# Kernel optimization log

Hardware: AMD Instinct MI355X
Metric: run time of the kernel (lower is better)

Reference implementation:

```python
import jax, jax.numpy as jnp
import numpy as np

HIDDEN = 64
N_NODES = 100000
N_EDGES = 1250000
EDGE_FEAT = 13


def setup_inputs() -> dict:
    key = jax.random.key(0)
    ks = jax.random.split(key, 16)
    d = HIDDEN
    inp = {
        'x': jax.random.normal(ks[0], (N_NODES, d), dtype=jnp.float32),
        'edge_index': jax.random.randint(ks[1], (2, N_EDGES), 0, N_NODES, dtype=jnp.int64),
        'edge_attr': jax.random.uniform(ks[2], (N_EDGES, EDGE_FEAT), dtype=jnp.float32),
        # learned params
        'aaaaa': jax.random.normal(ks[3], (EDGE_FEAT, 1), dtype=jnp.float32) * 0.5,
        'W1': jax.random.normal(ks[4], (d, d), dtype=jnp.float32) / np.sqrt(d),
        'b1': jnp.zeros((d,), dtype=jnp.float32),
        'W2': jax.random.normal(ks[5], (d, d), dtype=jnp.float32) / np.sqrt(d),
        'b2': jnp.zeros((d,), dtype=jnp.float32),
        'W3': jax.random.normal(ks[6], (d, d), dtype=jnp.float32) / np.sqrt(d),
        'b3': jnp.zeros((d,), dtype=jnp.float32),
        'wg1': jax.random.normal(ks[7], (d, 1), dtype=jnp.float32) / np.sqrt(d),
        'bg1': jnp.zeros((1,), dtype=jnp.float32),
        'wg2': jax.random.normal(ks[8], (d, 1), dtype=jnp.float32) / np.sqrt(d),
        'bg2': jnp.zeros((1,), dtype=jnp.float32),
        'wg3': jax.random.normal(ks[9], (d, 1), dtype=jnp.float32) / np.sqrt(d),
        'bg3': jnp.zeros((1,), dtype=jnp.float32),
    }
    return inp


def _gcn_norm(edge_index, edge_weight, num_nodes):
    # PyG gcn_norm: add self-loops (weight 1), symmetric deg^{-1/2} normalization
    loop = jnp.arange(num_nodes, dtype=edge_index.dtype)
    rows = jnp.concatenate([edge_index[0], loop])
    cols = jnp.concatenate([edge_index[1], loop])
    w = jnp.concatenate([edge_weight, jnp.ones((num_nodes,), edge_weight.dtype)])
    deg = jax.ops.segment_sum(w, cols, num_segments=num_nodes)
    dinv = jnp.where(deg > 0, jax.lax.rsqrt(jnp.where(deg > 0, deg, 1.0)), 0.0)
    norm = dinv[rows] * w * dinv[cols]
    return rows, cols, norm


def _gcn_layer(x, W, b, rows, cols, norm, num_nodes):
    h = x @ W  # transform first (out_dim == in_dim)
    msg = norm[:, None] * h[rows]          # gather + scale  [E+N, d]
    out = jnp.zeros_like(h).at[cols].add(msg)  # scatter-add aggregation
    return out + b


def _att_pool(x, wg, bg):
    # GlobalAttention with single graph (batch all zeros):
    # gate = sigmoid(Linear(x)); softmax over nodes; weighted sum
    gate = jax.nn.sigmoid(x @ wg + bg)      # [N, 1]
    a = jax.nn.softmax(gate, axis=0)        # softmax over node dim
    return jnp.sum(a * x, axis=0, keepdims=True)  # [1, d]


def reference(x, edge_index, edge_attr, aaaaa, W1, b1, W2, b2, W3, b3,
              wg1, bg1, wg2, bg2, wg3, bg3):
    num_nodes = x.shape[0]
    edge_weight = (edge_attr @ jax.nn.softmax(aaaaa, axis=0)).reshape(-1)  # [E]
    rows, cols, norm = _gcn_norm(edge_index, edge_weight, num_nodes)

    x1 = jax.nn.relu(_gcn_layer(x, W1, b1, rows, cols, norm, num_nodes))
    r1 = _att_pool(x1, wg1, bg1)
    x2 = jax.nn.relu(_gcn_layer(x1, W2, b2, rows, cols, norm, num_nodes))
    r2 = _att_pool(x2, wg2, bg2)
    x3 = jax.nn.relu(_gcn_layer(x2, W3, b3, rows, cols, norm, num_nodes))
    r3 = _att_pool(x3, wg3, bg3)
    return jnp.concatenate([r1, r2, r3], axis=1)  # [1, 3*hidden]
```

## Files before the change

### kernel.cpp

```cpp
#include <hip/hip_runtime.h>
#include <hip/hip_bf16.h>
#include <math.h>

#define HIDDEN    64
#define N_NODES   100000
#define N_EDGES   1250000
#define EDGE_FEAT 13

#define GATHER_BLOCKS 2048
#define GEMM_NB   ((N_NODES + 255) / 256)

#define NBKT    391
#define BCAP    4096
#define A_EPB   2048
#define NBLKA   ((N_EDGES + A_EPB - 1) / A_EPB)

typedef unsigned short bf16_t;
typedef unsigned char  u8;
typedef unsigned short u16;
typedef unsigned int   u32;
typedef unsigned long long u64;
typedef float f32x2 __attribute__((ext_vector_type(2)));

#if defined(__has_builtin)
# if __has_builtin(__builtin_amdgcn_cvt_f32_fp8)
#  define USE_HW_FP8 1
# endif
# if __has_builtin(__builtin_amdgcn_cvt_pk_f32_fp8)
#  define USE_HW_FP8PK 1
# endif
#endif

static __device__ __forceinline__ float bf2f(bf16_t u) {
    union { unsigned int i; float f; } x; x.i = ((unsigned int)u) << 16; return x.f;
}
static __device__ __forceinline__ bf16_t f2bf(float f) {
    union { float f; unsigned int i; } u; u.f = f;
    unsigned int r = u.i + 0x7FFFu + ((u.i >> 16) & 1u);
    return (bf16_t)(r >> 16);
}

static __device__ __forceinline__ u8 f2fp8(float f) {
    union { float f; unsigned int u; } v; v.f = f;
    unsigned int s = (v.u >> 31) << 7;
    unsigned int mag = v.u & 0x7fffffffu;
    if (mag >= 0x43E80000u) return (u8)(s | 0x7Eu);
    if (mag < 0x3C800000u) {
        union { unsigned int u; float f; } t; t.u = mag;
        int qi = (int)rintf(t.f * 512.0f);
        return (u8)(s | (unsigned int)qi);
    }
    unsigned int r = mag + 0x7FFFFu + ((mag >> 20) & 1u);
    unsigned int e8 = (r >> 23) - 120u;
    unsigned int m3 = (r >> 20) & 7u;
    return (u8)(s | (e8 << 3) | m3);
}

static __device__ __forceinline__ float fp8dec(u32 b) {
#ifdef USE_HW_FP8
    return __builtin_amdgcn_cvt_f32_fp8(b, 0);
#else
    u32 m = b & 0x7Fu;
    u32 sgn = (b & 0x80u) << 24;
    union { u32 u; float f; } fn; fn.u = 0x3C000000u + (m << 20);
    float mg = (m < 8u) ? (float)m * (1.0f / 512.0f) : fn.f;
    union { float f; u32 u; } r; r.f = mg; r.u |= sgn;
    return r.f;
#endif
}

static __device__ __forceinline__ void fp8x4dec(u32 w, float* f) {
#ifdef USE_HW_FP8PK
    f32x2 lo = __builtin_amdgcn_cvt_pk_f32_fp8(w, false);
    f32x2 hi = __builtin_amdgcn_cvt_pk_f32_fp8(w, true);
    f[0] = lo.x; f[1] = lo.y; f[2] = hi.x; f[3] = hi.y;
#else
    f[0] = fp8dec(w & 0xFFu);
    f[1] = fp8dec((w >> 8) & 0xFFu);
    f[2] = fp8dec((w >> 16) & 0xFFu);
    f[3] = fp8dec((w >> 24) & 0xFFu);
#endif
}

#define OFF_TOT    0
#define OFF_GBASE  2048
#define OFF_BLKH   4096
#define OFF_BLKE   960512
#define OFF_VST    1916928
#define OFF_START  1916928
#define OFF_DINV   2316928
#define OFF_ACC    2716928
#define OFF_POOLP  2717952
#define OFF_REC    4315392
#define OFF_H8     11916928
#define OFF_A      18316928
#define OFF_BREC   OFF_H8

__global__ __launch_bounds__(256) void wqk_kernel(
    const float* __restrict__ attr, const int* __restrict__ rows,
    const int* __restrict__ cols, const float* __restrict__ aaaaa,
    u64* __restrict__ vstash, int* __restrict__ blkHist, int E)
{
    __shared__ float s[16];
    __shared__ int hist[NBKT];
    __shared__ float astage[EDGE_FEAT * 256];
    int t = threadIdx.x, blk = blockIdx.x;
    if (t == 0) {
        float m = -1e30f;
        for (int i = 0; i < EDGE_FEAT; i++) m = fmaxf(m, aaaaa[i]);
        float ex[EDGE_FEAT]; float sum = 0.f;
        for (int i = 0; i < EDGE_FEAT; i++) { ex[i] = __expf(aaaaa[i] - m); sum += ex[i]; }
        float inv = 1.f / sum;
        for (int i = 0; i < EDGE_FEAT; i++) s[i] = ex[i] * inv;
    }
    for (int b = t; b < NBKT; b += 256) hist[b] = 0;
    __syncthreads();

    int e0 = blk * A_EPB;
#pragma unroll 1
    for (int c = 0; c < A_EPB / 256; c++) {
        int ebase = e0 + c * 256;
        int lim = (min(256, E - ebase)) * EDGE_FEAT;
        size_t gb = (size_t)ebase * EDGE_FEAT;
#pragma unroll
        for (int j = 0; j < EDGE_FEAT; j++) {
            int idx = t + j * 256;
            if (idx < lim) astage[idx] = attr[gb + idx];
        }
        __syncthreads();
        int e = ebase + t;
        if (e < E) {
            const float* rowp = &astage[t * EDGE_FEAT];
            float acc = 0.f;
#pragma unroll
            for (int f = 0; f < EDGE_FEAT; f++) acc = fmaf(rowp[f], s[f], acc);
            u32 wq = min((u32)(fmaxf(acc, 0.f) * 32768.0f), 32767u);
            u32 cc = (u32)cols[e], rr = (u32)rows[e];
            int rk = atomicAdd(&hist[cc >> 8], 1);
            vstash[e] = ((u64)(u32)rk << 49) | ((u64)wq << 34) | ((u64)cc << 17) | (u64)rr;
        }
        __syncthreads();
    }
    for (int b = t; b < NBKT; b += 256) blkHist[blk * NBKT + b] = hist[b];
}

__global__ __launch_bounds__(256) void colscan_kernel(
    const int* __restrict__ blkHist, int* __restrict__ blkExcl,
    int* __restrict__ bucketTot)
{
    __shared__ int sv[768];
    int t = threadIdx.x, b = blockIdx.x;
    int v0 = (t < NBLKA) ? blkHist[(size_t)t * NBKT + b] : 0;
    int v1 = (t + 256 < NBLKA) ? blkHist[(size_t)(t + 256) * NBKT + b] : 0;
    int v2 = (t + 512 < NBLKA) ? blkHist[(size_t)(t + 512) * NBKT + b] : 0;
    sv[t] = v0; sv[t + 256] = v1; sv[t + 512] = v2;
    __syncthreads();
    for (int off = 1; off < 768; off <<= 1) {
        int a0 = (t >= off) ? sv[t - off] : 0;
        int a1 = (t + 256 >= off) ? sv[t + 256 - off] : 0;
        int a2 = sv[t + 512 - off];
        __syncthreads();
        sv[t] += a0; sv[t + 256] += a1; sv[t + 512] += a2;
        __syncthreads();
    }
    if (t < NBLKA) blkExcl[(size_t)t * NBKT + b] = sv[t] - v0;
    if (t + 256 < NBLKA) blkExcl[(size_t)(t + 256) * NBKT + b] = sv[t + 256] - v1;
    if (t + 512 < NBLKA) blkExcl[(size_t)(t + 512) * NBKT + b] = sv[t + 512] - v2;
    if (t == 0) bucketTot[b] = sv[NBLKA - 1];
}

__global__ void bscan(const int* __restrict__ bucketTot, int* __restrict__ gbase) {
    __shared__ int sc[512];
    int t = threadIdx.x;
    int v0 = (t < NBKT) ? bucketTot[t] : 0;
    int v1 = (t + 256 < NBKT) ? bucketTot[t + 256] : 0;
    sc[t] = v0; sc[t + 256] = v1;
    __syncthreads();
    for (int off = 1; off < 512; off <<= 1) {
        int a0 = (t >= off) ? sc[t - off] : 0;
        int a1 = sc[t + 256 - off];
        __syncthreads();
        sc[t] += a0; sc[t + 256] += a1;
        __syncthreads();
    }
    if (t < NBKT) gbase[t] = sc[t] - v0;
    if (t + 256 < NBKT) gbase[t + 256] = sc[t + 256] - v1;
}

__global__ __launch_bounds__(256) void scat_kernel(
    const u64* __restrict__ vstash, const int* __restrict__ blkHist,
    const int* __restrict__ blkExcl, u64* __restrict__ brec, int E)
{
    __shared__ u64 lbuf[A_EPB];
    __shared__ int hist[NBKT];
    __shared__ int exg[NBKT];
    __shared__ int cex[512];
    int t = threadIdx.x, blk = blockIdx.x;
    for (int b = t; b < NBKT; b += 256) {
        hist[b] = blkHist[(size_t)blk * NBKT + b];
        exg[b]  = blkExcl[(size_t)blk * NBKT + b];
    }
    __syncthreads();
    cex[t]       = (t < NBKT) ? hist[t] : 0;
    cex[t + 256] = (t + 256 < NBKT) ? hist[t + 256] : 0;
    __syncthreads();
    for (int off = 1; off < 512; off <<= 1) {
        int a0 = (t >= off) ? cex[t - off] : 0;
        int a1 = cex[t + 256 - off];
        __syncthreads();
        cex[t] += a0; cex[t + 256] += a1;
        __syncthreads();
    }

    int e0 = blk * A_EPB;
    int blkcnt = min(A_EPB, E - e0);
    for (int c = 0; c < A_EPB / 256; c++) {
        int e = e0 + c * 256 + t;
        if (e < E) {
            u64 v = vstash[e];
            int b = (int)((v >> 25) & 0x1FFu);
            int rk = (int)(v >> 49);
            lbuf[cex[b] - hist[b] + rk] = v;
        }
    }
    __syncthreads();
    for (int i = t; i < blkcnt; i += 256) {
        u64 w = lbuf[i];
        int b = (int)((w >> 25) & 0x1FFu);
        int ex = cex[b] - hist[b];
        int slot = exg[b] + (i - ex);
        if (slot < BCAP)
            brec[(size_t)b * BCAP + slot] = w;
    }
}

__global__ __launch_bounds__(256) void sortb_kernel(
    const u64* __restrict__ brec,
    const int* __restrict__ bucketTot, const int* __restrict__ gbase,
    u32* __restrict__ recp, int* __restrict__ startA,
    float* __restrict__ dinv, int N)
{
    __shared__ int hist[256];
    __shared__ int isum[256];
    __shared__ int incl[256];
    __shared__ u16 rnk[BCAP];
    __shared__ u64 buf[BCAP];
    int t = threadIdx.x;
    int b = blockIdx.x;
    int cnt = min(bucketTot[b], BCAP);
    int gb = gbase[b];
    int cbase = b << 8;
    int ncols = min(256, N - cbase);
    hist[t] = 0; isum[t] = 0;
    __syncthreads();

    for (int i = t; i < cnt; i += 256) {
        u64 v = brec[(size_t)b * BCAP + i];
        buf[i] = v;
        int c = (int)((v >> 17) & 255u);
        int wq = (int)((v >> 34) & 0x7FFFu);
        rnk[i] = (u16)atomicAdd(&hist[c], 1);
        atomicAdd(&isum[c], wq);
    }
    __syncthreads();

    incl[t] = hist[t];
    __syncthreads();
    for (int off = 1; off < 256; off <<= 1) {
        int a0 = (t >= off) ? incl[t - off] : 0;
        __syncthreads();
        incl[t] += a0;
        __syncthreads();
    }
    if (t < ncols) {
        startA[cbase + t] = gb + (incl[t] - hist[t]);
        dinv[cbase + t] = rsqrtf(1.0f + (float)isum[t] * (1.0f / 32768.0f));
    }
    __syncthreads();

    for (int i = t; i < cnt; i += 256) {
        u64 v = buf[i];
        int c = (int)((v >> 17) & 255u);
        int ex = incl[c] - hist[c];
        u32 row = (u32)(v & 0x1FFFFu);
        u32 wq = (u32)((v >> 34) & 0x7FFFu);
        recp[gb + ex + rnk[i]] = (row << 15) | wq;
    }
}

template <typename T> struct Feat;
template <> struct Feat<float> {
    static __device__ __forceinline__ float4 ld4(const float* A, size_t off) {
        return *(const float4*)(A + off);
    }
};
template <> struct Feat<bf16_t> {
    static __device__ __forceinline__ float4 ld4(const bf16_t* A, size_t off) {
        uint2 v = *(const uint2*)(A + off);
        float4 r;
        r.x = bf2f((bf16_t)(v.x & 0xffffu));
        r.y = bf2f((bf16_t)(v.x >> 16));
        r.z = bf2f((bf16_t)(v.y & 0xffffu));
        r.w = bf2f((bf16_t)(v.y >> 16));
        return r;
    }
};

template <typename TIn>
__global__ __launch_bounds__(256) void gemm64(const TIn* __restrict__ A,
                                              const float* __restrict__ W,
                                              const float* __restrict__ dinv,
                                              u8* __restrict__ H8, int N) {
    __shared__ float Ws[HIDDEN * HIDDEN];
    int tid = threadIdx.x;
    {
        const float4* Wv = (const float4*)W;
        float4* Sv = (float4*)Ws;
#pragma unroll
        for (int i = 0; i < 4; i++) Sv[tid + 256 * i] = Wv[tid + 256 * i];
    }
    __syncthreads();
    int rg = tid >> 2;
    int c0 = (tid & 3) * 16;
    int rbase = blockIdx.x * 256 + rg;
    int rld[4]; bool rok[4];
#pragma unroll
    for (int i = 0; i < 4; i++) {
        int r = rbase + 64 * i;
        rok[i] = (r < N);
        rld[i] = rok[i] ? r : 0;
    }
    float acc[4][16];
#pragma unroll
    for (int i = 0; i < 4; i++)
#pragma unroll
        for (int j = 0; j < 16; j++) acc[i][j] = 0.f;

    for (int k = 0; k < HIDDEN; k += 4) {
        float4 a4[4];
#pragma unroll
        for (int i = 0; i < 4; i++)
            a4[i] = Feat<TIn>::ld4(A, (size_t)rld[i] * HIDDEN + k);
#pragma unroll
        for (int kk = 0; kk < 4; kk++) {
            const float* wr = &Ws[(k + kk) * HIDDEN + c0];
            float4 W0 = *(const float4*)(wr);
            float4 W1 = *(const float4*)(wr + 4);
            float4 W2 = *(const float4*)(wr + 8);
            float4 W3 = *(const float4*)(wr + 12);
            float wv[16] = {W0.x, W0.y, W0.z, W0.w, W1.x, W1.y, W1.z, W1.w,
                            W2.x, W2.y, W2.z, W2.w, W3.x, W3.y, W3.z, W3.w};
#pragma unroll
            for (int i = 0; i < 4; i++) {
                float ak[4] = {a4[i].x, a4[i].y, a4[i].z, a4[i].w};
                float av = ak[kk];
#pragma unroll
                for (int j = 0; j < 16; j++) acc[i][j] = fmaf(av, wv[j], acc[i][j]);
            }
        }
    }
#pragma unroll
    for (int i = 0; i < 4; i++) {
        if (!rok[i]) continue;
        float dv = dinv[rld[i]];
        unsigned int wd[4];
#pragma unroll
        for (int q = 0; q < 4; q++) {
            unsigned int b0 = f2fp8(dv * acc[i][4*q]);
            unsigned int b1 = f2fp8(dv * acc[i][4*q+1]);
            unsigned int b2 = f2fp8(dv * acc[i][4*q+2]);
            unsigned int b3 = f2fp8(dv * acc[i][4*q+3]);
            wd[q] = b0 | (b1 << 8) | (b2 << 16) | (b3 << 24);
        }
        *(uint4*)(H8 + (size_t)rld[i] * HIDDEN + c0) = make_uint4(wd[0], wd[1], wd[2], wd[3]);
    }
}

__global__ __launch_bounds__(256) void gather_pool_kernel(
    const u8* __restrict__ h8,
    const int* __restrict__ start,
    const u32* __restrict__ recp,
    const float* __restrict__ dinv, const float* __restrict__ bias,
    const float* __restrict__ wg, const float* __restrict__ bg,
    bf16_t* __restrict__ out, float* __restrict__ poolpart, int N)
{
    __shared__ float sred[4][65];
    int lane  = threadIdx.x & 63;
    int wid   = threadIdx.x >> 6;
    int eslot = lane >> 4;
    int ch4   = (lane & 15) * 4;
    int wave = blockIdx.x * 4 + wid;
    const int nwaves = GATHER_BLOCKS * 4;
    float4 wgv = *(const float4*)(wg + ch4);
    float4 bv4 = *(const float4*)(bias + ch4);
    float bg0 = bg[0];
    float accv[4] = {0.f, 0.f, 0.f, 0.f};
    float accs = 0.f;

    for (int n = wave; n < N; n += nwaves) {
        int s = start[n];
        int e2 = (n + 1 < N) ? start[n + 1] : N_EDGES;
        float di = dinv[n];
        float a[4] = {0.f, 0.f, 0.f, 0.f};
        for (int base = s; base < e2; base += 64) {
            int cnt64 = min(e2 - base, 64);
            u32 rv = recp[base + min(lane, cnt64 - 1)];
            for (int j = 0; j < cnt64; j += 8) {
                int q0 = j + eslot, q1 = j + 4 + eslot;
                u32 p0 = (u32)__shfl((int)rv, q0 & 63, 64);
                u32 p1 = (u32)__shfl((int)rv, q1 & 63, 64);
                float w0 = (q0 < cnt64) ? (float)(p0 & 0x7FFFu) : 0.f;
                float w1 = (q1 < cnt64) ? (float)(p1 & 0x7FFFu) : 0.f;
                u32 off0 = ((p0 & 0xFFFF8000u) >> 9) + (u32)ch4;
                u32 off1 = ((p1 & 0xFFFF8000u) >> 9) + (u32)ch4;
                u32 d0 = *(const u32*)(h8 + off0);
                u32 d1 = *(const u32*)(h8 + off1);
                float h0[4], h1[4];
                fp8x4dec(d0, h0);
                fp8x4dec(d1, h1);
#pragma unroll
                for (int i = 0; i < 4; i++) {
                    a[i] = fmaf(w0, h0[i], a[i]);
                    a[i] = fmaf(w1, h1[i], a[i]);
                }
            }
        }
#pragma unroll
        for (int i = 0; i < 4; i++) {
            a[i] += __shfl_xor(a[i], 16, 64);
            a[i] += __shfl_xor(a[i], 32, 64);
        }
        u32 sw = *(const u32*)(h8 + (u32)n * (u32)HIDDEN + (u32)ch4);
        float sf[4];
        fp8x4dec(sw, sf);
        float dis = di * (1.0f / 32768.0f);
        float v[4];
#pragma unroll
        for (int i = 0; i < 4; i++) {
            float t0 = fmaf(dis, a[i], ((const float*)&bv4)[i]);
            v[i] = fmaxf(fmaf(di, sf[i], t0), 0.f);
        }
        if (eslot == 0) {
            u32 lo = (u32)f2bf(v[0]) | ((u32)f2bf(v[1]) << 16);
            u32 hi = (u32)f2bf(v[2]) | ((u32)f2bf(v[3]) << 16);
            *(uint2*)(out + (size_t)n * HIDDEN + ch4) = make_uint2(lo, hi);
        }
        float p = v[0] * wgv.x + v[1] * wgv.y + v[2] * wgv.z + v[3] * wgv.w;
        p += __shfl_xor(p, 1, 64);
        p += __shfl_xor(p, 2, 64);
        p += __shfl_xor(p, 4, 64);
        p += __shfl_xor(p, 8, 64);
        float g = 1.f / (1.f + __expf(-(p + bg0)));
        float eg = __expf(g);
#pragma unroll
        for (int i = 0; i < 4; i++) accv[i] = fmaf(eg, v[i], accv[i]);
        accs += eg;
    }

    if (eslot == 0) {
        sred[wid][ch4 + 0] = accv[0];
        sred[wid][ch4 + 1] = accv[1];
        sred[wid][ch4 + 2] = accv[2];
        sred[wid][ch4 + 3] = accv[3];
    }
    if (lane == 0) sred[wid][64] = accs;
    __syncthreads();
    if (wid == 0) {
        float s0 = sred[0][lane] + sred[1][lane] + sred[2][lane] + sred[3][lane];
        poolpart[(size_t)lane * GATHER_BLOCKS + blockIdx.x] = s0;
        if (lane == 0) {
            float ss = sred[0][64] + sred[1][64] + sred[2][64] + sred[3][64];
            poolpart[(size_t)64 * GATHER_BLOCKS + blockIdx.x] = ss;
        }
    }
}

__global__ void pool_reduce(const float* __restrict__ poolpart, float* __restrict__ acc) {
    int entry = (int)((blockIdx.x * blockDim.x + threadIdx.x) >> 6);
    int lane = threadIdx.x & 63;
    if (entry >= 3 * 65) return;
    const float* p = poolpart + (size_t)entry * GATHER_BLOCKS;
    float s = 0.f;
    for (int i = lane; i < GATHER_BLOCKS; i += 64) s += p[i];
#pragma unroll
    for (int m = 32; m > 0; m >>= 1) s += __shfl_xor(s, m, 64);
    if (lane == 0) acc[entry] = s;
}

__global__ void finalize_kernel(const float* __restrict__ acc, float* __restrict__ out) {
    int i = threadIdx.x;
    if (i >= 3 * HIDDEN) return;
    int layer = i >> 6, c = i & 63;
    const float* a = acc + layer * 65;
    out[i] = a[c] / a[64];
}

extern "C" void kernel_launch(void* const* d_in, const int* in_sizes, int n_in,
                              void* d_out, int out_size, void* d_ws, size_t ws_size,
                              hipStream_t stream) {
    const float* x          = (const float*)d_in[0];
    const int*   edge_index = (const int*)  d_in[1];
    const float* edge_attr  = (const float*)d_in[2];
    const float* aaaaa      = (const float*)d_in[3];
    const float* W1 = (const float*)d_in[4];  const float* b1 = (const float*)d_in[5];
    const float* W2 = (const float*)d_in[6];  const float* b2 = (const float*)d_in[7];
    const float* W3 = (const float*)d_in[8];  const float* b3 = (const float*)d_in[9];
    const float* wg1 = (const float*)d_in[10]; const float* bg1 = (const float*)d_in[11];
    const float* wg2 = (const float*)d_in[12]; const float* bg2 = (const float*)d_in[13];
    const float* wg3 = (const float*)d_in[14]; const float* bg3 = (const float*)d_in[15];
    float* out = (float*)d_out;

    char* ws = (char*)d_ws;
    int*    bucketTot = (int*)   (ws + OFF_TOT);
    int*    gbase     = (int*)   (ws + OFF_GBASE);
    int*    blkHist   = (int*)   (ws + OFF_BLKH);
    int*    blkExcl   = (int*)   (ws + OFF_BLKE);
    u64*    vstash    = (u64*)   (ws + OFF_VST);
    int*    startA    = (int*)   (ws + OFF_START);
    float*  dinv      = (float*) (ws + OFF_DINV);
    float*  acc       = (float*) (ws + OFF_ACC);
    float*  poolpart  = (float*) (ws + OFF_POOLP);
    u32*    recp      = (u32*)   (ws + OFF_REC);
    u8*     h8        = (u8*)    (ws + OFF_H8);
    bf16_t* bufA      = (bf16_t*)(ws + OFF_A);
    u64*    brec      = (u64*)   (ws + OFF_BREC);

    const int* rows = edge_index;
    const int* cols = edge_index + N_EDGES;
    const int N = N_NODES, E = N_EDGES;

    wqk_kernel<<<NBLKA, 256, 0, stream>>>(edge_attr, rows, cols, aaaaa, vstash, blkHist, E);
    colscan_kernel<<<NBKT, 256, 0, stream>>>(blkHist, blkExcl, bucketTot);
    bscan<<<1, 256, 0, stream>>>(bucketTot, gbase);
    scat_kernel<<<NBLKA, 256, 0, stream>>>(vstash, blkHist, blkExcl, brec, E);
    sortb_kernel<<<NBKT, 256, 0, stream>>>(brec, bucketTot, gbase, recp, startA, dinv, N);

    const float* Wm[3]  = {W1, W2, W3};
    const float* bs[3]  = {b1, b2, b3};
    const float* wgs[3] = {wg1, wg2, wg3};
    const float* bgs[3] = {bg1, bg2, bg3};

    for (int l = 0; l < 3; l++) {
        if (l == 0)
            gemm64<float><<<GEMM_NB, 256, 0, stream>>>(x, Wm[l], dinv, h8, N);
        else
            gemm64<bf16_t><<<GEMM_NB, 256, 0, stream>>>(bufA, Wm[l], dinv, h8, N);
        gather_pool_kernel<<<GATHER_BLOCKS, 256, 0, stream>>>(
            h8, startA, recp, dinv, bs[l], wgs[l], bgs[l],
            bufA, poolpart + (size_t)l * 65 * GATHER_BLOCKS, N);
    }

    pool_reduce<<<(3 * 65 * 64 + 255) / 256, 256, 0, stream>>>(poolpart, acc);
    finalize_kernel<<<1, 192, 0, stream>>>(acc, out);
}
```

Before: 416.9 us.

## Halve edges per block, use per-wave attr staging, rewrite column scan

Each wave now stages its own 64-edge slice of edge attributes in its own shared-memory region. This removes the block-wide barriers inside the edge loop, and the softmax weights are kept in registers. Edges per block are halved, which doubles the block count and the per-block histogram storage, so the workspace offsets are shifted to fit. The column scan becomes a per-thread serial prefix over several blocks followed by a 256-wide block scan, so it handles the larger block count. The cost is more histogram traffic and a larger scan.

```diff
diff --git a/kernel.cpp b/kernel.cpp
--- a/kernel.cpp
+++ b/kernel.cpp
@@ -12,8 +12,9 @@
 
 #define NBKT    391
 #define BCAP    4096
-#define A_EPB   2048
+#define A_EPB   1024
 #define NBLKA   ((N_EDGES + A_EPB - 1) / A_EPB)
+#define CPT     ((NBLKA + 255) / 256)
 
 typedef unsigned short bf16_t;
 typedef unsigned char  u8;
@@ -85,15 +86,15 @@
 #define OFF_TOT    0
 #define OFF_GBASE  2048
 #define OFF_BLKH   4096
-#define OFF_BLKE   960512
-#define OFF_VST    1916928
-#define OFF_START  1916928
-#define OFF_DINV   2316928
-#define OFF_ACC    2716928
-#define OFF_POOLP  2717952
-#define OFF_REC    4315392
-#define OFF_H8     11916928
-#define OFF_A      18316928
+#define OFF_BLKE   1914880
+#define OFF_VST    3825664
+#define OFF_START  3825664
+#define OFF_DINV   4225664
+#define OFF_ACC    4625664
+#define OFF_POOLP  4626688
+#define OFF_REC    6224128
+#define OFF_H8     13825664
+#define OFF_A      20225664
 #define OFF_BREC   OFF_H8
 
 __global__ __launch_bounds__(256) void wqk_kernel(
@@ -103,8 +104,9 @@
 {
     __shared__ float s[16];
     __shared__ int hist[NBKT];
-    __shared__ float astage[EDGE_FEAT * 256];
+    __shared__ float astage[4][EDGE_FEAT * 64];
     int t = threadIdx.x, blk = blockIdx.x;
+    int lane = t & 63, wid = t >> 6;
     if (t == 0) {
         float m = -1e30f;
         for (int i = 0; i < EDGE_FEAT; i++) m = fmaxf(m, aaaaa[i]);
@@ -116,31 +118,37 @@
     for (int b = t; b < NBKT; b += 256) hist[b] = 0;
     __syncthreads();
 
-    int e0 = blk * A_EPB;
+    float sw[EDGE_FEAT];
+#pragma unroll
+    for (int f = 0; f < EDGE_FEAT; f++) sw[f] = s[f];
+
+    float* as = astage[wid];
+    int wbase = blk * A_EPB + wid * (A_EPB / 4);
 #pragma unroll 1
-    for (int c = 0; c < A_EPB / 256; c++) {
-        int ebase = e0 + c * 256;
-        int lim = (min(256, E - ebase)) * EDGE_FEAT;
+    for (int c = 0; c < A_EPB / 4 / 64; c++) {
+        int ebase = wbase + c * 64;
+        int rem = E - ebase;
+        if (rem <= 0) break;
+        int limw = min(64, rem) * EDGE_FEAT;
         size_t gb = (size_t)ebase * EDGE_FEAT;
 #pragma unroll
         for (int j = 0; j < EDGE_FEAT; j++) {
-            int idx = t + j * 256;
-            if (idx < lim) astage[idx] = attr[gb + idx];
-        }
-        __syncthreads();
-        int e = ebase + t;
+            int idx = lane + j * 64;
+            if (idx < limw) as[idx] = attr[gb + idx];
+        }
+        int e = ebase + lane;
         if (e < E) {
-            const float* rowp = &astage[t * EDGE_FEAT];
+            const float* rowp = &as[lane * EDGE_FEAT];
             float acc = 0.f;
 #pragma unroll
-            for (int f = 0; f < EDGE_FEAT; f++) acc = fmaf(rowp[f], s[f], acc);
+            for (int f = 0; f < EDGE_FEAT; f++) acc = fmaf(rowp[f], sw[f], acc);
             u32 wq = min((u32)(fmaxf(acc, 0.f) * 32768.0f), 32767u);
             u32 cc = (u32)cols[e], rr = (u32)rows[e];
             int rk = atomicAdd(&hist[cc >> 8], 1);
             vstash[e] = ((u64)(u32)rk << 49) | ((u64)wq << 34) | ((u64)cc << 17) | (u64)rr;
         }
-        __syncthreads();
-    }
+    }
+    __syncthreads();
     for (int b = t; b < NBKT; b += 256) blkHist[blk * NBKT + b] = hist[b];
 }
 
@@ -148,25 +156,30 @@
     const int* __restrict__ blkHist, int* __restrict__ blkExcl,
     int* __restrict__ bucketTot)
 {
-    __shared__ int sv[768];
+    __shared__ int sc[256];
     int t = threadIdx.x, b = blockIdx.x;
-    int v0 = (t < NBLKA) ? blkHist[(size_t)t * NBKT + b] : 0;
-    int v1 = (t + 256 < NBLKA) ? blkHist[(size_t)(t + 256) * NBKT + b] : 0;
-    int v2 = (t + 512 < NBLKA) ? blkHist[(size_t)(t + 512) * NBKT + b] : 0;
-    sv[t] = v0; sv[t + 256] = v1; sv[t + 512] = v2;
-    __syncthreads();
-    for (int off = 1; off < 768; off <<= 1) {
-        int a0 = (t >= off) ? sv[t - off] : 0;
-        int a1 = (t + 256 >= off) ? sv[t + 256 - off] : 0;
-        int a2 = sv[t + 512 - off];
-        __syncthreads();
-        sv[t] += a0; sv[t + 256] += a1; sv[t + 512] += a2;
-        __syncthreads();
-    }
-    if (t < NBLKA) blkExcl[(size_t)t * NBKT + b] = sv[t] - v0;
-    if (t + 256 < NBLKA) blkExcl[(size_t)(t + 256) * NBKT + b] = sv[t + 256] - v1;
-    if (t + 512 < NBLKA) blkExcl[(size_t)(t + 512) * NBKT + b] = sv[t + 512] - v2;
-    if (t == 0) bucketTot[b] = sv[NBLKA - 1];
+    int loc[CPT]; int lsum = 0;
+#pragma unroll
+    for (int i = 0; i < CPT; i++) {
+        int k = t * CPT + i;
+        int v = (k < NBLKA) ? blkHist[(size_t)k * NBKT + b] : 0;
+        loc[i] = lsum; lsum += v;
+    }
+    sc[t] = lsum;
+    __syncthreads();
+    for (int off = 1; off < 256; off <<= 1) {
+        int a = (t >= off) ? sc[t - off] : 0;
+        __syncthreads();
+        sc[t] += a;
+        __syncthreads();
+    }
+    int excl = sc[t] - lsum;
+#pragma unroll
+    for (int i = 0; i < CPT; i++) {
+        int k = t * CPT + i;
+        if (k < NBLKA) blkExcl[(size_t)k * NBKT + b] = excl + loc[i];
+    }
+    if (t == 255) bucketTot[b] = sc[255];
 }
 
 __global__ void bscan(const int* __restrict__ bucketTot, int* __restrict__ gbase) {
```

New measurement: 395.8 us. -5.1%, faster.
